# Kernel tuning notes

Hardware: AMD Instinct MI355X
Metric: run time of the kernel (lower is better)

## Reference

```python
import jax, jax.numpy as jnp
import numpy as np

N_MOL = 1024   # molecules
A = 16         # atoms per molecule
N = N_MOL * A  # 16384 atoms
E = N * A      # 262144 edges (all intra-molecule pairs incl. self, box side 2.5 < cutoff 5)
F = 128        # num_features
NRBF = 20
CUT = 5.0
EPS = 1e-8


def _lin(k, fan_in, fan_out):
    kw, kb = jax.random.split(k)
    s = 1.0 / np.sqrt(fan_in)
    return (jax.random.uniform(kw, (fan_in, fan_out), minval=-s, maxval=s),
            jax.random.uniform(kb, (fan_out,), minval=-s, maxval=s))


def setup_inputs() -> dict:
    key = jax.random.key(0)
    ks = jax.random.split(key, 12)
    atoms = jax.random.randint(ks[0], (N,), 0, 100)
    # coordinates in a box of side 2.5 per molecule -> all intra-molecule pairs within cutoff
    atom_positions = jax.random.uniform(ks[1], (N, 3), dtype=jnp.float32) * 2.5
    # deterministic edge list: for each atom i, all atoms j in the same molecule (incl. i itself)
    mol = np.arange(N) // A
    idx_i = jnp.asarray(np.repeat(np.arange(N), A).astype(np.int32))
    idx_j = jnp.asarray(((mol * A)[:, None] + np.arange(A)[None, :]).reshape(-1).astype(np.int32))
    embed = jax.random.normal(ks[2], (100, F), dtype=jnp.float32)
    w_s1, b_s1 = _lin(ks[3], F, F)
    w_s2, b_s2 = _lin(ks[4], F, 3 * F)
    w_r, b_r = _lin(ks[5], NRBF, 3 * F)
    w_u1, b_u1 = _lin(ks[6], 2 * F, F)
    w_u2, b_u2 = _lin(ks[7], F, 3 * F)
    def _lin3(k):
        ws, bs = zip(*[_lin(kk, F, F) for kk in jax.random.split(k, 3)])
        return jnp.stack(ws), jnp.stack(bs)
    Uw, Ub = _lin3(ks[8])   # [3,F,F], [3,F]
    Vw, Vb = _lin3(ks[9])
    return dict(atoms=atoms, atom_positions=atom_positions, idx_i=idx_i, idx_j=idx_j,
                embed=embed, w_s1=w_s1, b_s1=b_s1, w_s2=w_s2, b_s2=b_s2,
                w_r=w_r, b_r=b_r, w_u1=w_u1, b_u1=b_u1, w_u2=w_u2, b_u2=b_u2,
                Uw=Uw, Ub=Ub, Vw=Vw, Vb=Vb)


def reference(atoms, atom_positions, idx_i, idx_j, embed,
              w_s1, b_s1, w_s2, b_s2, w_r, b_r,
              w_u1, b_u1, w_u2, b_u2, Uw, Ub, Vw, Vb):
    silu = jax.nn.silu
    n_nodes = atoms.shape[0]
    s0 = embed[atoms]                                         # [N,F] (v0 is zeros -> its message term vanishes)
    # edge geometry: r_ij = pos_i - pos_j
    rvec = atom_positions[idx_i] - atom_positions[idx_j]      # [E,3]
    d = jnp.linalg.norm(rvec, axis=1, keepdims=True)          # [E,1]
    n = jnp.arange(1, NRBF + 1, dtype=s0.dtype)[None, :]      # [1,20]
    rbf = jnp.sin(n * (jnp.pi / CUT) * d) / (d + EPS)         # [E,20]
    lin_r = rbf @ w_r + b_r                                   # [E,3F]
    # cosine cutoff applied elementwise to the linear output (faithful to source)
    Wg = 0.5 * (jnp.cos(jnp.pi * lin_r / CUT) + 1.0) * (lin_r < CUT).astype(lin_r.dtype)
    phi = silu(s0 @ w_s1 + b_s1) @ w_s2 + b_s2                # [N,3F]
    split = phi[idx_j] * Wg                                   # [E,3F] gather + gate
    split_2 = split[:, F:2 * F]
    split_3 = split[:, 2 * F:]
    unit = rvec / (d + EPS)                                   # [E,3]
    # v_j[js]*split_1 term is identically zero since v_i_0 == 0
    left_2 = split_3[:, :, None] * unit[:, None, :]           # [E,F,3]
    v1 = jnp.zeros((n_nodes, F, 3), dtype=s0.dtype).at[idx_j].add(left_2)
    s1 = jnp.zeros((n_nodes, F), dtype=s0.dtype).at[idx_j].add(split_2)
    # update block: per-spatial-component linear maps
    Uv = jnp.einsum('nik,kio->nok', v1, Uw) + Ub.T[None]      # [N,F,3]
    Vv = jnp.einsum('nik,kio->nok', v1, Vw) + Vb.T[None]
    Vn = jnp.linalg.norm(Vv, axis=2)                          # [N,F]
    m = silu(jnp.concatenate([Vn, s1], axis=1) @ w_u1 + b_u1) @ w_u2 + b_u2
    a_vv, a_sv, a_ss = m[:, :F], m[:, F:2 * F], m[:, 2 * F:]
    delta_v = a_vv[:, :, None] * Uv                           # [N,F,3]
    delta_s = jnp.sum(Uv * Vv, axis=2) * a_sv + a_ss          # [N,F]
    return delta_s, delta_v
```

## Files before the change

kernel.cpp:

```cpp
#include <hip/hip_runtime.h>
#include <stdint.h>

#define N_ATOMS 16384
#define FDIM    128
#define NF      (N_ATOMS * FDIM)
#define PK      136

typedef __bf16 bf16;
typedef bf16  bf16x8 __attribute__((ext_vector_type(8)));
typedef float f32x4  __attribute__((ext_vector_type(4)));

#define MFMA(a, b, c) __builtin_amdgcn_mfma_f32_16x16x32_bf16((a), (b), (c), 0, 0, 0)

__device__ __forceinline__ float silu(float x) { return x / (1.0f + expf(-x)); }

__device__ __forceinline__ uint16_t f2b(float x) {
    union { float f; uint32_t u; } v; v.f = x;
    uint32_t r = (v.u + 0x7FFFu + ((v.u >> 16) & 1u)) >> 16;
    return (uint16_t)r;
}
__device__ __forceinline__ float b2f(uint16_t u) {
    return __uint_as_float(((uint32_t)u) << 16);
}

__device__ __forceinline__ float gate(float lin) {
    float x = lin * 0.1f;
    x = x - floorf(x);
    float cg = 0.5f * (__builtin_amdgcn_cosf(x) + 1.0f);
    return (lin < 5.0f) ? cg : 0.0f;
}

__device__ __forceinline__ void stage_w(uint16_t* bt, const uint16_t* __restrict__ src,
                                        int srcld, int t)
{
    #pragma unroll
    for (int g = 0; g < 8; ++g) {
        int idx = g * 256 + t;
        int n = idx >> 4, q = idx & 15;
        uint4 v = *(const uint4*)(src + (size_t)n * srcld + q * 8);
        *(uint4*)(bt + (size_t)n * PK + q * 8) = v;
    }
}

__global__ __launch_bounds__(256) void prep_kernel(
    const float* __restrict__ w_s1, const float* __restrict__ w_s2,
    const float* __restrict__ w_u1, const float* __restrict__ w_u2,
    const float* __restrict__ Uw,   const float* __restrict__ Vw,
    uint16_t* __restrict__ wb1,  uint16_t* __restrict__ wb2,
    uint16_t* __restrict__ wbu1, uint16_t* __restrict__ wbu2,
    uint16_t* __restrict__ Uwb,  uint16_t* __restrict__ Vwb)
{
    const int e = blockIdx.x * 256 + threadIdx.x;
    switch (blockIdx.y) {
    case 0: {
        if (e < 128 * 128) { int k = e & 127, n = e >> 7;
            wb1[e] = f2b(w_s1[k * 128 + n]); }
        break; }
    case 1: {
        if (e < 256 * 128) { int k = e & 127, n = e >> 7;
            wb2[e] = f2b(w_s2[k * 384 + 128 + n]); }
        break; }
    case 2: {
        if (e < 128 * 256) { int k = e & 255, n = e >> 8;
            wbu1[e] = f2b(w_u1[k * 128 + n]); }
        break; }
    case 3: {
        if (e < 384 * 128) { int k = e & 127, n = e >> 7;
            wbu2[e] = f2b(w_u2[k * 384 + n]); }
        break; }
    case 4: {
        if (e < 384 * 128) { int k = e & 127, n = e >> 7;
            Uwb[e] = f2b(Uw[(n >> 7) * 16384 + k * 128 + (n & 127)]); }
        break; }
    default: {
        if (e < 384 * 128) { int k = e & 127, n = e >> 7;
            Vwb[e] = f2b(Vw[(n >> 7) * 16384 + k * 128 + (n & 127)]); }
        break; }
    }
}

__global__ __launch_bounds__(256) void phi_kernel(
    const int* __restrict__ atoms,
    const float* __restrict__ embed,
    const uint16_t* __restrict__ wb1, const float* __restrict__ b1,
    const uint16_t* __restrict__ wb2, const float* __restrict__ b2,
    uint16_t* __restrict__ phi2)
{
    __shared__ uint16_t aS[64 * PK];
    __shared__ uint16_t bt[128 * PK];
    const int t = threadIdx.x;
    const int w = t >> 6, l = t & 63;
    const int lrow = l & 15, lk = (l >> 4) * 8;
    const int r0 = blockIdx.x * 64;

    {
        const int row = t & 63, ch = (t >> 6) * 32;
        const int aid = atoms[r0 + row];
        const float* src = embed + (size_t)aid * 128 + ch;
        #pragma unroll
        for (int g = 0; g < 4; ++g) {
            float4 v0 = ((const float4*)src)[2 * g];
            float4 v1 = ((const float4*)src)[2 * g + 1];
            union { uint16_t u16[8]; uint4 u4; } pk;
            pk.u16[0] = f2b(v0.x); pk.u16[1] = f2b(v0.y);
            pk.u16[2] = f2b(v0.z); pk.u16[3] = f2b(v0.w);
            pk.u16[4] = f2b(v1.x); pk.u16[5] = f2b(v1.y);
            pk.u16[6] = f2b(v1.z); pk.u16[7] = f2b(v1.w);
            *(uint4*)(aS + (size_t)row * PK + ch + 8 * g) = pk.u4;
        }
    }
    stage_w(bt, wb1, 128, t);
    __syncthreads();

    f32x4 acc1[8];
    #pragma unroll
    for (int n = 0; n < 8; ++n) acc1[n] = f32x4{0.f, 0.f, 0.f, 0.f};
    #pragma unroll
    for (int ks = 0; ks < 128; ks += 32) {
        bf16x8 af = *(const bf16x8*)(aS + (size_t)(16 * w + lrow) * PK + ks + lk);
        #pragma unroll
        for (int n = 0; n < 8; ++n) {
            bf16x8 bfr = *(const bf16x8*)(bt + (size_t)(16 * n + lrow) * PK + ks + lk);
            acc1[n] = MFMA(af, bfr, acc1[n]);
        }
    }
    #pragma unroll
    for (int n = 0; n < 8; ++n) {
        int col = 16 * n + lrow;
        float bb = b1[col];
        #pragma unroll
        for (int i = 0; i < 4; ++i) {
            int rl = 16 * w + (l >> 4) * 4 + i;
            aS[(size_t)rl * PK + col] = f2b(silu(acc1[n][i] + bb));
        }
    }

    for (int cc = 0; cc < 2; ++cc) {
        __syncthreads();
        stage_w(bt, wb2 + (size_t)(128 * cc) * 128, 128, t);
        __syncthreads();
        f32x4 acc[8];
        #pragma unroll
        for (int n = 0; n < 8; ++n) acc[n] = f32x4{0.f, 0.f, 0.f, 0.f};
        #pragma unroll
        for (int ks = 0; ks < 128; ks += 32) {
            bf16x8 af = *(const bf16x8*)(aS + (size_t)(16 * w + lrow) * PK + ks + lk);
            #pragma unroll
            for (int n = 0; n < 8; ++n) {
                bf16x8 bfr = *(const bf16x8*)(bt + (size_t)(16 * n + lrow) * PK + ks + lk);
                acc[n] = MFMA(af, bfr, acc[n]);
            }
        }
        #pragma unroll
        for (int n = 0; n < 8; ++n) {
            int col = 16 * n + lrow;
            float bb = b2[128 + 128 * cc + col];
            #pragma unroll
            for (int i = 0; i < 4; ++i) {
                int row = r0 + 16 * w + (l >> 4) * 4 + i;
                phi2[(size_t)row * 256 + 128 * cc + col] = f2b(acc[n][i] + bb);
            }
        }
    }
}

template <bool NEED_UNIT>
__device__ __forceinline__ void setup_mol(
    const float* __restrict__ pos, int mol0, int t,
    float (&rbf)[120][20], float (&unitv)[120][4],
    int (&pa)[120], int (&pb)[120], float (&posS)[16][3])
{
    if (t < 16) {
        posS[t][0] = pos[(mol0 + t) * 3 + 0];
        posS[t][1] = pos[(mol0 + t) * 3 + 1];
        posS[t][2] = pos[(mol0 + t) * 3 + 2];
    }
    if (t < 120) {
        int p = t;
        int b = (int)(0.5f * (1.0f + sqrtf(8.0f * (float)p + 1.0f)));
        while (b * (b - 1) / 2 > p) --b;
        while ((b + 1) * b / 2 <= p) ++b;
        pa[p] = p - b * (b - 1) / 2;
        pb[p] = b;
    }
    __syncthreads();
    if (t < 120) {
        int a = pa[t], b = pb[t];
        float dx = posS[a][0] - posS[b][0];
        float dy = posS[a][1] - posS[b][1];
        float dz = posS[a][2] - posS[b][2];
        float d = sqrtf(dx * dx + dy * dy + dz * dz);
        float inv = 1.0f / (d + 1e-8f);
        if (NEED_UNIT) {
            unitv[t][0] = dx * inv;
            unitv[t][1] = dy * inv;
            unitv[t][2] = dz * inv;
            unitv[t][3] = 0.f;
        }
        #pragma unroll
        for (int r = 0; r < 20; ++r) {
            float xr = (float)(r + 1) * d * 0.1f;
            xr = xr - floorf(xr);
            rbf[t][r] = __builtin_amdgcn_sinf(xr) * inv;
        }
    }
    __syncthreads();
}

__device__ __forceinline__ float pair_lin(const float (&rbf)[120][20],
                                          const float (&wr)[20], int p, float br)
{
    const float4* rb = (const float4*)&rbf[p][0];
    float lin = br;
    #pragma unroll
    for (int q = 0; q < 5; ++q) {
        float4 rv = rb[q];
        lin += rv.x * wr[4 * q] + rv.y * wr[4 * q + 1]
             + rv.z * wr[4 * q + 2] + rv.w * wr[4 * q + 3];
    }
    return lin;
}

__global__ __launch_bounds__(128) void edge_s2_kernel(
    const float* __restrict__ pos,
    const float* __restrict__ w_r, const float* __restrict__ b_r,
    const uint16_t* __restrict__ phi2,
    uint16_t* __restrict__ Xs)
{
    __shared__ float rbf[120][20];
    __shared__ float unitv[120][4];
    __shared__ int pa[120], pb[120];
    __shared__ float posS[16][3];
    const int t = threadIdx.x;
    const int mol0 = blockIdx.x * 16;
    setup_mol<false>(pos, mol0, t, rbf, unitv, pa, pb, posS);

    const int c = 128 + t;
    float wr[20];
    #pragma unroll
    for (int r = 0; r < 20; ++r) wr[r] = w_r[r * 384 + c];
    const float br = b_r[c];

    float acc[16];
    const float wg0 = gate(br);
    #pragma unroll
    for (int a = 0; a < 16; ++a) acc[a] = wg0;

    #pragma unroll
    for (int b = 1; b < 16; ++b) {
        #pragma unroll
        for (int a = 0; a < b; ++a) {
            const int p = b * (b - 1) / 2 + a;
            float Wg = gate(pair_lin(rbf, wr, p, br));
            acc[a] += Wg;
            acc[b] += Wg;
        }
    }

    #pragma unroll
    for (int a = 0; a < 16; ++a) {
        Xs[(size_t)(mol0 + a) * 128 + t] =
            f2b(b2f(phi2[(size_t)(mol0 + a) * 256 + t]) * acc[a]);
    }
}

__global__ __launch_bounds__(128) void edge_s3_kernel(
    const float* __restrict__ pos,
    const float* __restrict__ w_r, const float* __restrict__ b_r,
    const uint16_t* __restrict__ phi2,
    uint16_t* __restrict__ v1)
{
    __shared__ float rbf[120][20];
    __shared__ float unitv[120][4];
    __shared__ int pa[120], pb[120];
    __shared__ float posS[16][3];
    const int t = threadIdx.x;
    const int mol0 = blockIdx.x * 16;
    setup_mol<true>(pos, mol0, t, rbf, unitv, pa, pb, posS);

    const int c = 256 + t;
    float wr[20];
    #pragma unroll
    for (int r = 0; r < 20; ++r) wr[r] = w_r[r * 384 + c];
    const float br = b_r[c];

    float sx[16], sy[16], sz[16];
    #pragma unroll
    for (int a = 0; a < 16; ++a) { sx[a] = 0.f; sy[a] = 0.f; sz[a] = 0.f; }

    #pragma unroll
    for (int b = 1; b < 16; ++b) {
        #pragma unroll
        for (int a = 0; a < b; ++a) {
            const int p = b * (b - 1) / 2 + a;
            float Wg = gate(pair_lin(rbf, wr, p, br));
            float4 u = *(const float4*)&unitv[p][0];
            float gx = Wg * u.x, gy = Wg * u.y, gz = Wg * u.z;
            sx[b] += gx; sy[b] += gy; sz[b] += gz;
            sx[a] -= gx; sy[a] -= gy; sz[a] -= gz;
        }
    }

    #pragma unroll
    for (int a = 0; a < 16; ++a) {
        float p3 = b2f(phi2[(size_t)(mol0 + a) * 256 + 128 + t]);
        size_t base = (size_t)(mol0 + a) * 128 + t;
        v1[base]                  = f2b(p3 * sx[a]);
        v1[(size_t)NF + base]     = f2b(p3 * sy[a]);
        v1[2 * (size_t)NF + base] = f2b(p3 * sz[a]);
    }
}

__global__ __launch_bounds__(256) void uv_kernel(
    const uint16_t* __restrict__ v1,
    const uint16_t* __restrict__ Uwb, const float* __restrict__ Ub,
    const uint16_t* __restrict__ Vwb, const float* __restrict__ Vb,
    uint16_t* __restrict__ Uvb, uint16_t* __restrict__ Vvb)
{
    __shared__ uint16_t bt[128 * PK];
    const int y = blockIdx.y;
    const int k = y % 3;
    const bool isV = (y >= 3);
    const uint16_t* Bw  = (isV ? Vwb : Uwb) + (size_t)k * 16384;
    const float*   bias = (isV ? Vb : Ub) + k * 128;
    const uint16_t* A = v1 + (size_t)k * NF;
    uint16_t* out = (isV ? Vvb : Uvb) + (size_t)k * NF;

    const int t = threadIdx.x;
    const int w = t >> 6, l = t & 63;
    const int lrow = l & 15, lk = (l >> 4) * 8;
    const int r0 = blockIdx.x * 64;

    stage_w(bt, Bw, 128, t);
    __syncthreads();

    f32x4 acc[8];
    #pragma unroll
    for (int n = 0; n < 8; ++n) acc[n] = f32x4{0.f, 0.f, 0.f, 0.f};

    #pragma unroll
    for (int ks = 0; ks < 128; ks += 32) {
        bf16x8 af = *(const bf16x8*)(A + (size_t)(r0 + 16 * w + lrow) * 128 + ks + lk);
        #pragma unroll
        for (int n = 0; n < 8; ++n) {
            bf16x8 bfr = *(const bf16x8*)(bt + (size_t)(16 * n + lrow) * PK + ks + lk);
            acc[n] = MFMA(af, bfr, acc[n]);
        }
    }

    #pragma unroll
    for (int n = 0; n < 8; ++n) {
        int col = 16 * n + lrow;
        float bb = bias[col];
        #pragma unroll
        for (int i = 0; i < 4; ++i) {
            int row = r0 + 16 * w + (l >> 4) * 4 + i;
            out[(size_t)row * 128 + col] = f2b(acc[n][i] + bb);
        }
    }
}

__global__ __launch_bounds__(256) void update_kernel(
    const uint16_t* __restrict__ Xs,
    const uint16_t* __restrict__ wbu1, const float* __restrict__ b_u1,
    const uint16_t* __restrict__ wbu2, const float* __restrict__ b_u2,
    const uint16_t* __restrict__ Uvb, const uint16_t* __restrict__ Vvb,
    float* __restrict__ out)
{
    __shared__ uint16_t bt[128 * PK];
    __shared__ uint16_t hS[64 * PK];
    const int t = threadIdx.x;
    const int w = t >> 6, l = t & 63;
    const int lrow = l & 15, lk = (l >> 4) * 8;
    const int r0 = blockIdx.x * 64;

    f32x4 acc1[8];
    #pragma unroll
    for (int n = 0; n < 8; ++n) acc1[n] = f32x4{0.f, 0.f, 0.f, 0.f};

    stage_w(bt, wbu1 + 0, 256, t);
    __syncthreads();
    #pragma unroll
    for (int ks = 0; ks < 128; ks += 32) {
        size_t base = (size_t)(r0 + 16 * w + lrow) * 128 + ks + lk;
        uint4 A0 = *(const uint4*)(Vvb + base);
        uint4 A1 = *(const uint4*)(Vvb + (size_t)NF + base);
        uint4 A2 = *(const uint4*)(Vvb + 2 * (size_t)NF + base);
        const uint16_t* p0 = (const uint16_t*)&A0;
        const uint16_t* p1 = (const uint16_t*)&A1;
        const uint16_t* p2 = (const uint16_t*)&A2;
        union { uint16_t u16[8]; bf16x8 v; } af;
        #pragma unroll
        for (int j = 0; j < 8; ++j) {
            float x0 = b2f(p0[j]), x1 = b2f(p1[j]), x2 = b2f(p2[j]);
            af.u16[j] = f2b(sqrtf(x0 * x0 + x1 * x1 + x2 * x2));
        }
        #pragma unroll
        for (int n = 0; n < 8; ++n) {
            bf16x8 bfr = *(const bf16x8*)(bt + (size_t)(16 * n + lrow) * PK + ks + lk);
            acc1[n] = MFMA(af.v, bfr, acc1[n]);
        }
    }

    __syncthreads();
    stage_w(bt, wbu1 + 128, 256, t);
    __syncthreads();
    #pragma unroll
    for (int ks = 0; ks < 128; ks += 32) {
        bf16x8 af = *(const bf16x8*)(Xs + (size_t)(r0 + 16 * w + lrow) * 128 + ks + lk);
        #pragma unroll
        for (int n = 0; n < 8; ++n) {
            bf16x8 bfr = *(const bf16x8*)(bt + (size_t)(16 * n + lrow) * PK + ks + lk);
            acc1[n] = MFMA(af, bfr, acc1[n]);
        }
    }

    #pragma unroll
    for (int n = 0; n < 8; ++n) {
        int col = 16 * n + lrow;
        float bb = b_u1[col];
        #pragma unroll
        for (int i = 0; i < 4; ++i) {
            int rl = 16 * w + (l >> 4) * 4 + i;
            hS[(size_t)rl * PK + col] = f2b(silu(acc1[n][i] + bb));
        }
    }

    f32x4 macc[3][8];
    for (int cc = 0; cc < 3; ++cc) {
        __syncthreads();
        stage_w(bt, wbu2 + (size_t)(128 * cc) * 128, 128, t);
        __syncthreads();
        #pragma unroll
        for (int n = 0; n < 8; ++n) macc[cc][n] = f32x4{0.f, 0.f, 0.f, 0.f};
        #pragma unroll
        for (int ks = 0; ks < 128; ks += 32) {
            bf16x8 af = *(const bf16x8*)(hS + (size_t)(16 * w + lrow) * PK + ks + lk);
            #pragma unroll
            for (int n = 0; n < 8; ++n) {
                bf16x8 bfr = *(const bf16x8*)(bt + (size_t)(16 * n + lrow) * PK + ks + lk);
                macc[cc][n] = MFMA(af, bfr, macc[cc][n]);
            }
        }
    }

    float* dv = out + (size_t)NF;
    #pragma unroll
    for (int n = 0; n < 8; ++n) {
        int f = 16 * n + lrow;
        float bvv = b_u2[f], bsv = b_u2[128 + f], bss = b_u2[256 + f];
        #pragma unroll
        for (int i = 0; i < 4; ++i) {
            int row = r0 + 16 * w + (l >> 4) * 4 + i;
            float a_vv = macc[0][n][i] + bvv;
            float a_sv = macc[1][n][i] + bsv;
            float a_ss = macc[2][n][i] + bss;
            size_t base = (size_t)row * 128 + f;
            float u0 = b2f(Uvb[base]);
            float u1 = b2f(Uvb[(size_t)NF + base]);
            float u2 = b2f(Uvb[2 * (size_t)NF + base]);
            float v0 = b2f(Vvb[base]);
            float v1 = b2f(Vvb[(size_t)NF + base]);
            float v2 = b2f(Vvb[2 * (size_t)NF + base]);
            out[base] = (u0 * v0 + u1 * v1 + u2 * v2) * a_sv + a_ss;
            size_t o = base * 3;
            dv[o + 0] = a_vv * u0;
            dv[o + 1] = a_vv * u1;
            dv[o + 2] = a_vv * u2;
        }
    }
}

extern "C" void kernel_launch(void* const* d_in, const int* in_sizes, int n_in,
                              void* d_out, int out_size, void* d_ws, size_t ws_size,
                              hipStream_t stream)
{
    const int*   atoms = (const int*)d_in[0];
    const float* pos   = (const float*)d_in[1];
    const float* embed = (const float*)d_in[4];
    const float* w_s1  = (const float*)d_in[5];
    const float* b_s1  = (const float*)d_in[6];
    const float* w_s2  = (const float*)d_in[7];
    const float* b_s2  = (const float*)d_in[8];
    const float* w_r   = (const float*)d_in[9];
    const float* b_r   = (const float*)d_in[10];
    const float* w_u1  = (const float*)d_in[11];
    const float* b_u1  = (const float*)d_in[12];
    const float* w_u2  = (const float*)d_in[13];
    const float* b_u2  = (const float*)d_in[14];
    const float* Uw    = (const float*)d_in[15];
    const float* Ub    = (const float*)d_in[16];
    const float* Vw    = (const float*)d_in[17];
    const float* Vb    = (const float*)d_in[18];

    uint16_t* phi2 = (uint16_t*)d_ws;
    uint16_t* Xs   = phi2 + (size_t)N_ATOMS * 256;
    uint16_t* v1b  = Xs   + (size_t)NF;
    uint16_t* Uvb  = v1b  + 3ull * NF;
    uint16_t* Vvb  = Uvb  + 3ull * NF;
    uint16_t* wb1  = Vvb  + 3ull * NF;
    uint16_t* wb2  = wb1  + 128 * 128;
    uint16_t* wbu1 = wb2  + 256 * 128;
    uint16_t* wbu2 = wbu1 + 128 * 256;
    uint16_t* Uwb  = wbu2 + 384 * 128;
    uint16_t* Vwb  = Uwb  + 384 * 128;

    prep_kernel<<<dim3(192, 6), 256, 0, stream>>>(w_s1, w_s2, w_u1, w_u2, Uw, Vw,
                                                  wb1, wb2, wbu1, wbu2, Uwb, Vwb);
    phi_kernel<<<N_ATOMS / 64, 256, 0, stream>>>(atoms, embed, wb1, b_s1, wb2, b_s2, phi2);
    edge_s2_kernel<<<N_ATOMS / 16, 128, 0, stream>>>(pos, w_r, b_r, phi2, Xs);
    edge_s3_kernel<<<N_ATOMS / 16, 128, 0, stream>>>(pos, w_r, b_r, phi2, v1b);
    uv_kernel<<<dim3(N_ATOMS / 64, 6), 256, 0, stream>>>(v1b, Uwb, Ub, Vwb, Vb, Uvb, Vvb);
    update_kernel<<<N_ATOMS / 64, 256, 0, stream>>>(Xs, wbu1, b_u1, wbu2, b_u2, Uvb, Vvb, (float*)d_out);
}
```

Before: 202.8 us.

## Merge edge s2/s3 kernels and halve row tiles in phi and update GEMMs

Combines the two per-molecule edge kernels into one 256-thread kernel, where the first half of the threads computes the scalar-gate sums and the second half the vector sums. This shares the rbf/unit-vector setup and saves a launch. The phi and update kernels now tile 32 rows per block with a 2x2 warp grid instead of 64 rows with 1x4, doubling the block count for better occupancy and load balance, at the cost of restaging the weights twice as often. In the merged edge kernel every thread computes all four accumulators, so each thread does extra work that the other half then discards.

```diff
diff --git a/kernel.cpp b/kernel.cpp
--- a/kernel.cpp
+++ b/kernel.cpp
@@ -86,19 +86,21 @@
     const uint16_t* __restrict__ wb2, const float* __restrict__ b2,
     uint16_t* __restrict__ phi2)
 {
-    __shared__ uint16_t aS[64 * PK];
+    __shared__ uint16_t aS[32 * PK];
     __shared__ uint16_t bt[128 * PK];
     const int t = threadIdx.x;
     const int w = t >> 6, l = t & 63;
-    const int lrow = l & 15, lk = (l >> 4) * 8;
-    const int r0 = blockIdx.x * 64;
+    const int lrow = l & 15, quad = l >> 4, lk = quad * 8;
+    const int rowg = w & 1, colg = w >> 1;
+    const int r0 = blockIdx.x * 32;
 
     {
-        const int row = t & 63, ch = (t >> 6) * 32;
+        const int row = t >> 3;
+        const int ch  = (t & 7) * 16;
         const int aid = atoms[r0 + row];
         const float* src = embed + (size_t)aid * 128 + ch;
         #pragma unroll
-        for (int g = 0; g < 4; ++g) {
+        for (int g = 0; g < 2; ++g) {
             float4 v0 = ((const float4*)src)[2 * g];
             float4 v1 = ((const float4*)src)[2 * g + 1];
             union { uint16_t u16[8]; uint4 u4; } pk;
@@ -112,25 +114,25 @@
     stage_w(bt, wb1, 128, t);
     __syncthreads();
 
-    f32x4 acc1[8];
-    #pragma unroll
-    for (int n = 0; n < 8; ++n) acc1[n] = f32x4{0.f, 0.f, 0.f, 0.f};
+    f32x4 acc1[4];
+    #pragma unroll
+    for (int n = 0; n < 4; ++n) acc1[n] = f32x4{0.f, 0.f, 0.f, 0.f};
     #pragma unroll
     for (int ks = 0; ks < 128; ks += 32) {
-        bf16x8 af = *(const bf16x8*)(aS + (size_t)(16 * w + lrow) * PK + ks + lk);
-        #pragma unroll
-        for (int n = 0; n < 8; ++n) {
-            bf16x8 bfr = *(const bf16x8*)(bt + (size_t)(16 * n + lrow) * PK + ks + lk);
+        bf16x8 af = *(const bf16x8*)(aS + (size_t)(16 * rowg + lrow) * PK + ks + lk);
+        #pragma unroll
+        for (int n = 0; n < 4; ++n) {
+            bf16x8 bfr = *(const bf16x8*)(bt + (size_t)(64 * colg + 16 * n + lrow) * PK + ks + lk);
             acc1[n] = MFMA(af, bfr, acc1[n]);
         }
     }
     #pragma unroll
-    for (int n = 0; n < 8; ++n) {
-        int col = 16 * n + lrow;
+    for (int n = 0; n < 4; ++n) {
+        int col = 64 * colg + 16 * n + lrow;
         float bb = b1[col];
         #pragma unroll
         for (int i = 0; i < 4; ++i) {
-            int rl = 16 * w + (l >> 4) * 4 + i;
+            int rl = 16 * rowg + quad * 4 + i;
             aS[(size_t)rl * PK + col] = f2b(silu(acc1[n][i] + bb));
         }
     }
@@ -139,32 +141,31 @@
         __syncthreads();
         stage_w(bt, wb2 + (size_t)(128 * cc) * 128, 128, t);
         __syncthreads();
-        f32x4 acc[8];
-        #pragma unroll
-        for (int n = 0; n < 8; ++n) acc[n] = f32x4{0.f, 0.f, 0.f, 0.f};
+        f32x4 acc[4];
+        #pragma unroll
+        for (int n = 0; n < 4; ++n) acc[n] = f32x4{0.f, 0.f, 0.f, 0.f};
         #pragma unroll
         for (int ks = 0; ks < 128; ks += 32) {
-            bf16x8 af = *(const bf16x8*)(aS + (size_t)(16 * w + lrow) * PK + ks + lk);
+            bf16x8 af = *(const bf16x8*)(aS + (size_t)(16 * rowg + lrow) * PK + ks + lk);
             #pragma unroll
-            for (int n = 0; n < 8; ++n) {
-                bf16x8 bfr = *(const bf16x8*)(bt + (size_t)(16 * n + lrow) * PK + ks + lk);
+            for (int n = 0; n < 4; ++n) {
+                bf16x8 bfr = *(const bf16x8*)(bt + (size_t)(64 * colg + 16 * n + lrow) * PK + ks + lk);
                 acc[n] = MFMA(af, bfr, acc[n]);
             }
         }
         #pragma unroll
-        for (int n = 0; n < 8; ++n) {
-            int col = 16 * n + lrow;
+        for (int n = 0; n < 4; ++n) {
+            int col = 64 * colg + 16 * n + lrow;
             float bb = b2[128 + 128 * cc + col];
             #pragma unroll
             for (int i = 0; i < 4; ++i) {
-                int row = r0 + 16 * w + (l >> 4) * 4 + i;
+                int row = r0 + 16 * rowg + quad * 4 + i;
                 phi2[(size_t)row * 256 + 128 * cc + col] = f2b(acc[n][i] + bb);
             }
         }
     }
 }
 
-template <bool NEED_UNIT>
 __device__ __forceinline__ void setup_mol(
     const float* __restrict__ pos, int mol0, int t,
     float (&rbf)[120][20], float (&unitv)[120][4],
@@ -191,12 +192,10 @@
         float dz = posS[a][2] - posS[b][2];
         float d = sqrtf(dx * dx + dy * dy + dz * dz);
         float inv = 1.0f / (d + 1e-8f);
-        if (NEED_UNIT) {
-            unitv[t][0] = dx * inv;
-            unitv[t][1] = dy * inv;
-            unitv[t][2] = dz * inv;
-            unitv[t][3] = 0.f;
-        }
+        unitv[t][0] = dx * inv;
+        unitv[t][1] = dy * inv;
+        unitv[t][2] = dz * inv;
+        unitv[t][3] = 0.f;
         #pragma unroll
         for (int r = 0; r < 20; ++r) {
             float xr = (float)(r + 1) * d * 0.1f;
@@ -221,11 +220,12 @@
     return lin;
 }
 
-__global__ __launch_bounds__(128) void edge_s2_kernel(
+__global__ __launch_bounds__(256) void edge_kernel(
     const float* __restrict__ pos,
     const float* __restrict__ w_r, const float* __restrict__ b_r,
     const uint16_t* __restrict__ phi2,
-    uint16_t* __restrict__ Xs)
+    uint16_t* __restrict__ Xs,
+    uint16_t* __restrict__ v1)
 {
     __shared__ float rbf[120][20];
     __shared__ float unitv[120][4];
@@ -233,60 +233,18 @@
     __shared__ float posS[16][3];
     const int t = threadIdx.x;
     const int mol0 = blockIdx.x * 16;
-    setup_mol<false>(pos, mol0, t, rbf, unitv, pa, pb, posS);
+    setup_mol(pos, mol0, t, rbf, unitv, pa, pb, posS);
 
     const int c = 128 + t;
     float wr[20];
     #pragma unroll
     for (int r = 0; r < 20; ++r) wr[r] = w_r[r * 384 + c];
     const float br = b_r[c];
-
-    float acc[16];
-    const float wg0 = gate(br);
-    #pragma unroll
-    for (int a = 0; a < 16; ++a) acc[a] = wg0;
-
-    #pragma unroll
-    for (int b = 1; b < 16; ++b) {
-        #pragma unroll
-        for (int a = 0; a < b; ++a) {
-            const int p = b * (b - 1) / 2 + a;
-            float Wg = gate(pair_lin(rbf, wr, p, br));
-            acc[a] += Wg;
-            acc[b] += Wg;
-        }
-    }
-
-    #pragma unroll
-    for (int a = 0; a < 16; ++a) {
-        Xs[(size_t)(mol0 + a) * 128 + t] =
-            f2b(b2f(phi2[(size_t)(mol0 + a) * 256 + t]) * acc[a]);
-    }
-}
-
-__global__ __launch_bounds__(128) void edge_s3_kernel(
-    const float* __restrict__ pos,
-    const float* __restrict__ w_r, const float* __restrict__ b_r,
-    const uint16_t* __restrict__ phi2,
-    uint16_t* __restrict__ v1)
-{
-    __shared__ float rbf[120][20];
-    __shared__ float unitv[120][4];
-    __shared__ int pa[120], pb[120];
-    __shared__ float posS[16][3];
-    const int t = threadIdx.x;
-    const int mol0 = blockIdx.x * 16;
-    setup_mol<true>(pos, mol0, t, rbf, unitv, pa, pb, posS);
-
-    const int c = 256 + t;
-    float wr[20];
-    #pragma unroll
-    for (int r = 0; r < 20; ++r) wr[r] = w_r[r * 384 + c];
-    const float br = b_r[c];
-
-    float sx[16], sy[16], sz[16];
-    #pragma unroll
-    for (int a = 0; a < 16; ++a) { sx[a] = 0.f; sy[a] = 0.f; sz[a] = 0.f; }
+    const float m = (t < 128) ? 0.f : 1.f;
+
+    float aS[16], aX[16], aY[16], aZ[16];
+    #pragma unroll
+    for (int a = 0; a < 16; ++a) { aS[a] = 0.f; aX[a] = 0.f; aY[a] = 0.f; aZ[a] = 0.f; }
 
     #pragma unroll
     for (int b = 1; b < 16; ++b) {
@@ -295,19 +253,29 @@
             const int p = b * (b - 1) / 2 + a;
             float Wg = gate(pair_lin(rbf, wr, p, br));
             float4 u = *(const float4*)&unitv[p][0];
-            float gx = Wg * u.x, gy = Wg * u.y, gz = Wg * u.z;
-            sx[b] += gx; sy[b] += gy; sz[b] += gz;
-            sx[a] -= gx; sy[a] -= gy; sz[a] -= gz;
-        }
-    }
-
-    #pragma unroll
-    for (int a = 0; a < 16; ++a) {
-        float p3 = b2f(phi2[(size_t)(mol0 + a) * 256 + 128 + t]);
-        size_t base = (size_t)(mol0 + a) * 128 + t;
-        v1[base]                  = f2b(p3 * sx[a]);
-        v1[(size_t)NF + base]     = f2b(p3 * sy[a]);
-        v1[2 * (size_t)NF + base] = f2b(p3 * sz[a]);
+            float gx = Wg * (m * u.x), gy = Wg * (m * u.y), gz = Wg * (m * u.z);
+            aS[b] += Wg;  aX[b] += gx; aY[b] += gy; aZ[b] += gz;
+            aS[a] += Wg;  aX[a] -= gx; aY[a] -= gy; aZ[a] -= gz;
+        }
+    }
+
+    if (t < 128) {
+        const float wg0 = gate(br);
+        #pragma unroll
+        for (int a = 0; a < 16; ++a) {
+            Xs[(size_t)(mol0 + a) * 128 + t] =
+                f2b(b2f(phi2[(size_t)(mol0 + a) * 256 + t]) * (aS[a] + wg0));
+        }
+    } else {
+        const int f = t - 128;
+        #pragma unroll
+        for (int a = 0; a < 16; ++a) {
+            float p3 = b2f(phi2[(size_t)(mol0 + a) * 256 + 128 + f]);
+            size_t base = (size_t)(mol0 + a) * 128 + f;
+            v1[base]                  = f2b(p3 * aX[a]);
+            v1[(size_t)NF + base]     = f2b(p3 * aY[a]);
+            v1[2 * (size_t)NF + base] = f2b(p3 * aZ[a]);
+        }
     }
 }
 
@@ -328,7 +296,7 @@
 
     const int t = threadIdx.x;
     const int w = t >> 6, l = t & 63;
-    const int lrow = l & 15, lk = (l >> 4) * 8;
+    const int lrow = l & 15, quad = l >> 4, lk = quad * 8;
     const int r0 = blockIdx.x * 64;
 
     stage_w(bt, Bw, 128, t);
@@ -354,7 +322,7 @@
         float bb = bias[col];
         #pragma unroll
         for (int i = 0; i < 4; ++i) {
-            int row = r0 + 16 * w + (l >> 4) * 4 + i;
+            int row = r0 + 16 * w + quad * 4 + i;
             out[(size_t)row * 128 + col] = f2b(acc[n][i] + bb);
         }
     }
@@ -368,21 +336,22 @@
     float* __restrict__ out)
 {
     __shared__ uint16_t bt[128 * PK];
-    __shared__ uint16_t hS[64 * PK];
+    __shared__ uint16_t hS[32 * PK];
     const int t = threadIdx.x;
     const int w = t >> 6, l = t & 63;
-    const int lrow = l & 15, lk = (l >> 4) * 8;
-    const int r0 = blockIdx.x * 64;
-
-    f32x4 acc1[8];
-    #pragma unroll
-    for (int n = 0; n < 8; ++n) acc1[n] = f32x4{0.f, 0.f, 0.f, 0.f};
+    const int lrow = l & 15, quad = l >> 4, lk = quad * 8;
+    const int rowg = w & 1, colg = w >> 1;
+    const int r0 = blockIdx.x * 32;
+
+    f32x4 acc1[4];
+    #pragma unroll
+    for (int n = 0; n < 4; ++n) acc1[n] = f32x4{0.f, 0.f, 0.f, 0.f};
 
     stage_w(bt, wbu1 + 0, 256, t);
     __syncthreads();
     #pragma unroll
     for (int ks = 0; ks < 128; ks += 32) {
-        size_t base = (size_t)(r0 + 16 * w + lrow) * 128 + ks + lk;
+        size_t base = (size_t)(r0 + 16 * rowg + lrow) * 128 + ks + lk;
         uint4 A0 = *(const uint4*)(Vvb + base);
         uint4 A1 = *(const uint4*)(Vvb + (size_t)NF + base);
         uint4 A2 = *(const uint4*)(Vvb + 2 * (size_t)NF + base);
@@ -396,8 +365,8 @@
             af.u16[j] = f2b(sqrtf(x0 * x0 + x1 * x1 + x2 * x2));
         }
         #pragma unroll
-        for (int n = 0; n < 8; ++n) {
-            bf16x8 bfr = *(const bf16x8*)(bt + (size_t)(16 * n + lrow) * PK + ks + lk);
+        for (int n = 0; n < 4; ++n) {
+            bf16x8 bfr = *(const bf16x8*)(bt + (size_t)(64 * colg + 16 * n + lrow) * PK + ks + lk);
             acc1[n] = MFMA(af.v, bfr, acc1[n]);
         }
     }
@@ -407,38 +376,38 @@
     __syncthreads();
     #pragma unroll
     for (int ks = 0; ks < 128; ks += 32) {
-        bf16x8 af = *(const bf16x8*)(Xs + (size_t)(r0 + 16 * w + lrow) * 128 + ks + lk);
-        #pragma unroll
-        for (int n = 0; n < 8; ++n) {
-            bf16x8 bfr = *(const bf16x8*)(bt + (size_t)(16 * n + lrow) * PK + ks + lk);
+        bf16x8 af = *(const bf16x8*)(Xs + (size_t)(r0 + 16 * rowg + lrow) * 128 + ks + lk);
+        #pragma unroll
+        for (int n = 0; n < 4; ++n) {
+            bf16x8 bfr = *(const bf16x8*)(bt + (size_t)(64 * colg + 16 * n + lrow) * PK + ks + lk);
             acc1[n] = MFMA(af, bfr, acc1[n]);
         }
     }
 
     #pragma unroll
-    for (int n = 0; n < 8; ++n) {
-        int col = 16 * n + lrow;
+    for (int n = 0; n < 4; ++n) {
+        int col = 64 * colg + 16 * n + lrow;
         float bb = b_u1[col];
         #pragma unroll
         for (int i = 0; i < 4; ++i) {
-            int rl = 16 * w + (l >> 4) * 4 + i;
+            int rl = 16 * rowg + quad * 4 + i;
             hS[(size_t)rl * PK + col] = f2b(silu(acc1[n][i] + bb));
         }
     }
 
-    f32x4 macc[3][8];
+    f32x4 macc[3][4];
     for (int cc = 0; cc < 3; ++cc) {
         __syncthreads();
         stage_w(bt, wbu2 + (size_t)(128 * cc) * 128, 128, t);
         __syncthreads();
         #pragma unroll
-        for (int n = 0; n < 8; ++n) macc[cc][n] = f32x4{0.f, 0.f, 0.f, 0.f};
+        for (int n = 0; n < 4; ++n) macc[cc][n] = f32x4{0.f, 0.f, 0.f, 0.f};
         #pragma unroll
         for (int ks = 0; ks < 128; ks += 32) {
-            bf16x8 af = *(const bf16x8*)(hS + (size_t)(16 * w + lrow) * PK + ks + lk);
+            bf16x8 af = *(const bf16x8*)(hS + (size_t)(16 * rowg + lrow) * PK + ks + lk);
             #pragma unroll
-            for (int n = 0; n < 8; ++n) {
-                bf16x8 bfr = *(const bf16x8*)(bt + (size_t)(16 * n + lrow) * PK + ks + lk);
+            for (int n = 0; n < 4; ++n) {
+                bf16x8 bfr = *(const bf16x8*)(bt + (size_t)(64 * colg + 16 * n + lrow) * PK + ks + lk);
                 macc[cc][n] = MFMA(af, bfr, macc[cc][n]);
             }
         }
@@ -446,12 +415,12 @@
 
     float* dv = out + (size_t)NF;
     #pragma unroll
-    for (int n = 0; n < 8; ++n) {
-        int f = 16 * n + lrow;
+    for (int n = 0; n < 4; ++n) {
+        int f = 64 * colg + 16 * n + lrow;
         float bvv = b_u2[f], bsv = b_u2[128 + f], bss = b_u2[256 + f];
         #pragma unroll
         for (int i = 0; i < 4; ++i) {
-            int row = r0 + 16 * w + (l >> 4) * 4 + i;
+            int row = r0 + 16 * rowg + quad * 4 + i;
             float a_vv = macc[0][n][i] + bvv;
             float a_sv = macc[1][n][i] + bsv;
             float a_ss = macc[2][n][i] + bss;
@@ -507,9 +476,8 @@
 
     prep_kernel<<<dim3(192, 6), 256, 0, stream>>>(w_s1, w_s2, w_u1, w_u2, Uw, Vw,
                                                   wb1, wb2, wbu1, wbu2, Uwb, Vwb);
-    phi_kernel<<<N_ATOMS / 64, 256, 0, stream>>>(atoms, embed, wb1, b_s1, wb2, b_s2, phi2);
-    edge_s2_kernel<<<N_ATOMS / 16, 128, 0, stream>>>(pos, w_r, b_r, phi2, Xs);
-    edge_s3_kernel<<<N_ATOMS / 16, 128, 0, stream>>>(pos, w_r, b_r, phi2, v1b);
+    phi_kernel<<<N_ATOMS / 32, 256, 0, stream>>>(atoms, embed, wb1, b_s1, wb2, b_s2, phi2);
+    edge_kernel<<<N_ATOMS / 16, 256, 0, stream>>>(pos, w_r, b_r, phi2, Xs, v1b);
     uv_kernel<<<dim3(N_ATOMS / 64, 6), 256, 0, stream>>>(v1b, Uwb, Ub, Vwb, Vb, Uvb, Vvb);
-    update_kernel<<<N_ATOMS / 64, 256, 0, stream>>>(Xs, wbu1, b_u1, wbu2, b_u2, Uvb, Vvb, (float*)d_out);
-}
+    update_kernel<<<N_ATOMS / 32, 256, 0, stream>>>(Xs, wbu1, b_u1, wbu2, b_u2, Uvb, Vvb, (float*)d_out);
+}
```

After: 238.4 us. 17.6% more time.

## Fuse edge kernels and compute radial filter and aggregation with MFMA

Applied to the files above, without the earlier changes.

Replaces the two scalar per-feature edge kernels with one fused kernel. Each block builds a bf16 RBF tile per molecule, computes the gated filter for all 120 pairs with MFMA, and performs the per-atom scatter-add of the scalar and vector messages as a second MFMA against a ±1/unit-vector aggregation matrix. This trades scalar FMA work, duplicated geometry setup and an extra launch for tensor-core matmuls. The cost is more bf16 rounding in the filter and in the aggregation coefficients, plus larger shared memory use per block.

```diff
diff --git a/kernel.cpp b/kernel.cpp
--- a/kernel.cpp
+++ b/kernel.cpp
@@ -46,9 +46,11 @@
     const float* __restrict__ w_s1, const float* __restrict__ w_s2,
     const float* __restrict__ w_u1, const float* __restrict__ w_u2,
     const float* __restrict__ Uw,   const float* __restrict__ Vw,
+    const float* __restrict__ w_r,
     uint16_t* __restrict__ wb1,  uint16_t* __restrict__ wb2,
     uint16_t* __restrict__ wbu1, uint16_t* __restrict__ wbu2,
-    uint16_t* __restrict__ Uwb,  uint16_t* __restrict__ Vwb)
+    uint16_t* __restrict__ Uwb,  uint16_t* __restrict__ Vwb,
+    uint16_t* __restrict__ wrbt)
 {
     const int e = blockIdx.x * 256 + threadIdx.x;
     switch (blockIdx.y) {
@@ -72,9 +74,13 @@
         if (e < 384 * 128) { int k = e & 127, n = e >> 7;
             Uwb[e] = f2b(Uw[(n >> 7) * 16384 + k * 128 + (n & 127)]); }
         break; }
-    default: {
+    case 5: {
         if (e < 384 * 128) { int k = e & 127, n = e >> 7;
             Vwb[e] = f2b(Vw[(n >> 7) * 16384 + k * 128 + (n & 127)]); }
+        break; }
+    default: {
+        if (e < 256 * 32) { int k = e & 31, n = e >> 5;
+            wrbt[e] = (k < 20) ? f2b(w_r[k * 384 + 128 + n]) : (uint16_t)0; }
         break; }
     }
 }
@@ -90,7 +96,7 @@
     __shared__ uint16_t bt[128 * PK];
     const int t = threadIdx.x;
     const int w = t >> 6, l = t & 63;
-    const int lrow = l & 15, lk = (l >> 4) * 8;
+    const int lrow = l & 15, quad = l >> 4, lk = quad * 8;
     const int r0 = blockIdx.x * 64;
 
     {
@@ -130,7 +136,7 @@
         float bb = b1[col];
         #pragma unroll
         for (int i = 0; i < 4; ++i) {
-            int rl = 16 * w + (l >> 4) * 4 + i;
+            int rl = 16 * w + quad * 4 + i;
             aS[(size_t)rl * PK + col] = f2b(silu(acc1[n][i] + bb));
         }
     }
@@ -157,157 +163,148 @@
             float bb = b2[128 + 128 * cc + col];
             #pragma unroll
             for (int i = 0; i < 4; ++i) {
-                int row = r0 + 16 * w + (l >> 4) * 4 + i;
+                int row = r0 + 16 * w + quad * 4 + i;
                 phi2[(size_t)row * 256 + 128 * cc + col] = f2b(acc[n][i] + bb);
             }
         }
     }
 }
 
-template <bool NEED_UNIT>
-__device__ __forceinline__ void setup_mol(
-    const float* __restrict__ pos, int mol0, int t,
-    float (&rbf)[120][20], float (&unitv)[120][4],
-    int (&pa)[120], int (&pb)[120], float (&posS)[16][3])
-{
+__global__ __launch_bounds__(256) void edge_kernel(
+    const float* __restrict__ pos,
+    const uint16_t* __restrict__ wrbt,
+    const float* __restrict__ b_r,
+    const uint16_t* __restrict__ phi2,
+    uint16_t* __restrict__ Xs,
+    uint16_t* __restrict__ v1)
+{
+    __shared__ uint16_t rbf_bt[128 * 40];
+    __shared__ uint16_t WgA[128 * PK];
+    __shared__ uint16_t agg[64 * PK];
+    __shared__ float posS[16][3];
+
+    const int t = threadIdx.x;
+    const int w = t >> 6, l = t & 63;
+    const int lrow = l & 15, quad = l >> 4;
+    const int mol0 = blockIdx.x * 16;
+    const uint16_t ONE = 0x3F80;
+
     if (t < 16) {
         posS[t][0] = pos[(mol0 + t) * 3 + 0];
         posS[t][1] = pos[(mol0 + t) * 3 + 1];
         posS[t][2] = pos[(mol0 + t) * 3 + 2];
     }
+    for (int idx = t; idx < 64 * PK / 8; idx += 256)
+        ((uint4*)agg)[idx] = uint4{0, 0, 0, 0};
+    __syncthreads();
+
     if (t < 120) {
         int p = t;
         int b = (int)(0.5f * (1.0f + sqrtf(8.0f * (float)p + 1.0f)));
         while (b * (b - 1) / 2 > p) --b;
         while ((b + 1) * b / 2 <= p) ++b;
-        pa[p] = p - b * (b - 1) / 2;
-        pb[p] = b;
-    }
-    __syncthreads();
-    if (t < 120) {
-        int a = pa[t], b = pb[t];
+        int a = p - b * (b - 1) / 2;
         float dx = posS[a][0] - posS[b][0];
         float dy = posS[a][1] - posS[b][1];
         float dz = posS[a][2] - posS[b][2];
         float d = sqrtf(dx * dx + dy * dy + dz * dz);
         float inv = 1.0f / (d + 1e-8f);
-        if (NEED_UNIT) {
-            unitv[t][0] = dx * inv;
-            unitv[t][1] = dy * inv;
-            unitv[t][2] = dz * inv;
-            unitv[t][3] = 0.f;
-        }
+        float ux = dx * inv, uy = dy * inv, uz = dz * inv;
+
+        union { uint16_t u16[40]; uint4 u4[5]; } row;
         #pragma unroll
         for (int r = 0; r < 20; ++r) {
             float xr = (float)(r + 1) * d * 0.1f;
             xr = xr - floorf(xr);
-            rbf[t][r] = __builtin_amdgcn_sinf(xr) * inv;
-        }
-    }
-    __syncthreads();
-}
-
-__device__ __forceinline__ float pair_lin(const float (&rbf)[120][20],
-                                          const float (&wr)[20], int p, float br)
-{
-    const float4* rb = (const float4*)&rbf[p][0];
-    float lin = br;
-    #pragma unroll
-    for (int q = 0; q < 5; ++q) {
-        float4 rv = rb[q];
-        lin += rv.x * wr[4 * q] + rv.y * wr[4 * q + 1]
-             + rv.z * wr[4 * q + 2] + rv.w * wr[4 * q + 3];
-    }
-    return lin;
-}
-
-__global__ __launch_bounds__(128) void edge_s2_kernel(
-    const float* __restrict__ pos,
-    const float* __restrict__ w_r, const float* __restrict__ b_r,
-    const uint16_t* __restrict__ phi2,
-    uint16_t* __restrict__ Xs)
-{
-    __shared__ float rbf[120][20];
-    __shared__ float unitv[120][4];
-    __shared__ int pa[120], pb[120];
-    __shared__ float posS[16][3];
-    const int t = threadIdx.x;
-    const int mol0 = blockIdx.x * 16;
-    setup_mol<false>(pos, mol0, t, rbf, unitv, pa, pb, posS);
-
-    const int c = 128 + t;
-    float wr[20];
-    #pragma unroll
-    for (int r = 0; r < 20; ++r) wr[r] = w_r[r * 384 + c];
-    const float br = b_r[c];
-
-    float acc[16];
-    const float wg0 = gate(br);
-    #pragma unroll
-    for (int a = 0; a < 16; ++a) acc[a] = wg0;
-
-    #pragma unroll
-    for (int b = 1; b < 16; ++b) {
-        #pragma unroll
-        for (int a = 0; a < b; ++a) {
-            const int p = b * (b - 1) / 2 + a;
-            float Wg = gate(pair_lin(rbf, wr, p, br));
-            acc[a] += Wg;
-            acc[b] += Wg;
-        }
-    }
-
-    #pragma unroll
-    for (int a = 0; a < 16; ++a) {
-        Xs[(size_t)(mol0 + a) * 128 + t] =
-            f2b(b2f(phi2[(size_t)(mol0 + a) * 256 + t]) * acc[a]);
-    }
-}
-
-__global__ __launch_bounds__(128) void edge_s3_kernel(
-    const float* __restrict__ pos,
-    const float* __restrict__ w_r, const float* __restrict__ b_r,
-    const uint16_t* __restrict__ phi2,
-    uint16_t* __restrict__ v1)
-{
-    __shared__ float rbf[120][20];
-    __shared__ float unitv[120][4];
-    __shared__ int pa[120], pb[120];
-    __shared__ float posS[16][3];
-    const int t = threadIdx.x;
-    const int mol0 = blockIdx.x * 16;
-    setup_mol<true>(pos, mol0, t, rbf, unitv, pa, pb, posS);
-
-    const int c = 256 + t;
-    float wr[20];
-    #pragma unroll
-    for (int r = 0; r < 20; ++r) wr[r] = w_r[r * 384 + c];
-    const float br = b_r[c];
-
-    float sx[16], sy[16], sz[16];
-    #pragma unroll
-    for (int a = 0; a < 16; ++a) { sx[a] = 0.f; sy[a] = 0.f; sz[a] = 0.f; }
-
-    #pragma unroll
-    for (int b = 1; b < 16; ++b) {
-        #pragma unroll
-        for (int a = 0; a < b; ++a) {
-            const int p = b * (b - 1) / 2 + a;
-            float Wg = gate(pair_lin(rbf, wr, p, br));
-            float4 u = *(const float4*)&unitv[p][0];
-            float gx = Wg * u.x, gy = Wg * u.y, gz = Wg * u.z;
-            sx[b] += gx; sy[b] += gy; sz[b] += gz;
-            sx[a] -= gx; sy[a] -= gy; sz[a] -= gz;
-        }
-    }
-
-    #pragma unroll
-    for (int a = 0; a < 16; ++a) {
-        float p3 = b2f(phi2[(size_t)(mol0 + a) * 256 + 128 + t]);
-        size_t base = (size_t)(mol0 + a) * 128 + t;
-        v1[base]                  = f2b(p3 * sx[a]);
-        v1[(size_t)NF + base]     = f2b(p3 * sy[a]);
-        v1[2 * (size_t)NF + base] = f2b(p3 * sz[a]);
+            row.u16[r] = f2b(__builtin_amdgcn_sinf(xr) * inv);
+        }
+        #pragma unroll
+        for (int r = 20; r < 40; ++r) row.u16[r] = 0;
+        #pragma unroll
+        for (int g = 0; g < 5; ++g) ((uint4*)(rbf_bt + p * 40))[g] = row.u4[g];
+
+        agg[(0 * 16 + a) * PK + p] = ONE;
+        agg[(0 * 16 + b) * PK + p] = ONE;
+        agg[(16 + a) * PK + p] = f2b(-ux);  agg[(16 + b) * PK + p] = f2b(ux);
+        agg[(32 + a) * PK + p] = f2b(-uy);  agg[(32 + b) * PK + p] = f2b(uy);
+        agg[(48 + a) * PK + p] = f2b(-uz);  agg[(48 + b) * PK + p] = f2b(uz);
+    } else if (t < 128) {
+        #pragma unroll
+        for (int g = 0; g < 5; ++g) ((uint4*)(rbf_bt + t * 40))[g] = uint4{0, 0, 0, 0};
+    } else if (t < 144) {
+        agg[(t - 128) * PK + 120] = ONE;
+    }
+    __syncthreads();
+
+    for (int cc = 0; cc < 2; ++cc) {
+        const uint16_t* wA = wrbt + (size_t)(cc * 128) * 32;
+        #pragma unroll
+        for (int ft2 = 0; ft2 < 2; ++ft2) {
+            const int ft = 2 * w + ft2;
+            bf16x8 afr = *(const bf16x8*)(wA + (size_t)(ft * 16 + lrow) * 32 + quad * 8);
+            float brv[4];
+            #pragma unroll
+            for (int i = 0; i < 4; ++i)
+                brv[i] = b_r[128 + cc * 128 + ft * 16 + quad * 4 + i];
+            #pragma unroll
+            for (int pt = 0; pt < 8; ++pt) {
+                bf16x8 bfr = *(const bf16x8*)(rbf_bt + (size_t)(pt * 16 + lrow) * 40 + quad * 8);
+                f32x4 c = MFMA(afr, bfr, (f32x4{0.f, 0.f, 0.f, 0.f}));
+                #pragma unroll
+                for (int i = 0; i < 4; ++i) {
+                    int f = ft * 16 + quad * 4 + i;
+                    int p = pt * 16 + lrow;
+                    WgA[(size_t)f * PK + p] = f2b(gate(c[i] + brv[i]));
+                }
+            }
+        }
+
+        const int ntiles = cc ? 3 : 1;
+        const int nbase  = cc ? 16 : 0;
+        f32x4 acc[2][3];
+        #pragma unroll
+        for (int ft2 = 0; ft2 < 2; ++ft2)
+            #pragma unroll
+            for (int nt = 0; nt < 3; ++nt) acc[ft2][nt] = f32x4{0.f, 0.f, 0.f, 0.f};
+
+        #pragma unroll
+        for (int ks = 0; ks < 128; ks += 32) {
+            bf16x8 a0 = *(const bf16x8*)(WgA + (size_t)((2 * w) * 16 + lrow) * PK + ks + quad * 8);
+            bf16x8 a1 = *(const bf16x8*)(WgA + (size_t)((2 * w + 1) * 16 + lrow) * PK + ks + quad * 8);
+            for (int nt = 0; nt < ntiles; ++nt) {
+                bf16x8 bfr = *(const bf16x8*)(agg + (size_t)(nbase + nt * 16 + lrow) * PK + ks + quad * 8);
+                acc[0][nt] = MFMA(a0, bfr, acc[0][nt]);
+                acc[1][nt] = MFMA(a1, bfr, acc[1][nt]);
+            }
+        }
+
+        const int a = lrow;
+        #pragma unroll
+        for (int ft2 = 0; ft2 < 2; ++ft2) {
+            const int fbase = (2 * w + ft2) * 16 + quad * 4;
+            float ph[4];
+            #pragma unroll
+            for (int i = 0; i < 4; ++i)
+                ph[i] = b2f(phi2[(size_t)(mol0 + a) * 256 + cc * 128 + fbase + i]);
+            if (cc == 0) {
+                ushort4 ov;
+                ov.x = f2b(ph[0] * acc[ft2][0][0]);
+                ov.y = f2b(ph[1] * acc[ft2][0][1]);
+                ov.z = f2b(ph[2] * acc[ft2][0][2]);
+                ov.w = f2b(ph[3] * acc[ft2][0][3]);
+                *(ushort4*)(Xs + (size_t)(mol0 + a) * 128 + fbase) = ov;
+            } else {
+                #pragma unroll
+                for (int nt = 0; nt < 3; ++nt) {
+                    ushort4 ov;
+                    ov.x = f2b(ph[0] * acc[ft2][nt][0]);
+                    ov.y = f2b(ph[1] * acc[ft2][nt][1]);
+                    ov.z = f2b(ph[2] * acc[ft2][nt][2]);
+                    ov.w = f2b(ph[3] * acc[ft2][nt][3]);
+                    *(ushort4*)(v1 + (size_t)nt * NF + (size_t)(mol0 + a) * 128 + fbase) = ov;
+                }
+            }
+        }
     }
 }
 
@@ -328,7 +325,7 @@
 
     const int t = threadIdx.x;
     const int w = t >> 6, l = t & 63;
-    const int lrow = l & 15, lk = (l >> 4) * 8;
+    const int lrow = l & 15, quad = l >> 4, lk = quad * 8;
     const int r0 = blockIdx.x * 64;
 
     stage_w(bt, Bw, 128, t);
@@ -354,7 +351,7 @@
         float bb = bias[col];
         #pragma unroll
         for (int i = 0; i < 4; ++i) {
-            int row = r0 + 16 * w + (l >> 4) * 4 + i;
+            int row = r0 + 16 * w + quad * 4 + i;
             out[(size_t)row * 128 + col] = f2b(acc[n][i] + bb);
         }
     }
@@ -371,7 +368,7 @@
     __shared__ uint16_t hS[64 * PK];
     const int t = threadIdx.x;
     const int w = t >> 6, l = t & 63;
-    const int lrow = l & 15, lk = (l >> 4) * 8;
+    const int lrow = l & 15, quad = l >> 4, lk = quad * 8;
     const int r0 = blockIdx.x * 64;
 
     f32x4 acc1[8];
@@ -421,7 +418,7 @@
         float bb = b_u1[col];
         #pragma unroll
         for (int i = 0; i < 4; ++i) {
-            int rl = 16 * w + (l >> 4) * 4 + i;
+            int rl = 16 * w + quad * 4 + i;
             hS[(size_t)rl * PK + col] = f2b(silu(acc1[n][i] + bb));
         }
     }
@@ -451,7 +448,7 @@
         float bvv = b_u2[f], bsv = b_u2[128 + f], bss = b_u2[256 + f];
         #pragma unroll
         for (int i = 0; i < 4; ++i) {
-            int row = r0 + 16 * w + (l >> 4) * 4 + i;
+            int row = r0 + 16 * w + quad * 4 + i;
             float a_vv = macc[0][n][i] + bvv;
             float a_sv = macc[1][n][i] + bsv;
             float a_ss = macc[2][n][i] + bss;
@@ -504,12 +501,12 @@
     uint16_t* wbu2 = wbu1 + 128 * 256;
     uint16_t* Uwb  = wbu2 + 384 * 128;
     uint16_t* Vwb  = Uwb  + 384 * 128;
-
-    prep_kernel<<<dim3(192, 6), 256, 0, stream>>>(w_s1, w_s2, w_u1, w_u2, Uw, Vw,
-                                                  wb1, wb2, wbu1, wbu2, Uwb, Vwb);
+    uint16_t* wrbt = Vwb  + 384 * 128;
+
+    prep_kernel<<<dim3(192, 7), 256, 0, stream>>>(w_s1, w_s2, w_u1, w_u2, Uw, Vw, w_r,
+                                                  wb1, wb2, wbu1, wbu2, Uwb, Vwb, wrbt);
     phi_kernel<<<N_ATOMS / 64, 256, 0, stream>>>(atoms, embed, wb1, b_s1, wb2, b_s2, phi2);
-    edge_s2_kernel<<<N_ATOMS / 16, 128, 0, stream>>>(pos, w_r, b_r, phi2, Xs);
-    edge_s3_kernel<<<N_ATOMS / 16, 128, 0, stream>>>(pos, w_r, b_r, phi2, v1b);
+    edge_kernel<<<N_ATOMS / 16, 256, 0, stream>>>(pos, wrbt, b_r, phi2, Xs, v1b);
     uv_kernel<<<dim3(N_ATOMS / 64, 6), 256, 0, stream>>>(v1b, Uwb, Ub, Vwb, Vb, Uvb, Vvb);
     update_kernel<<<N_ATOMS / 64, 256, 0, stream>>>(Xs, wbu1, b_u1, wbu2, b_u2, Uvb, Vvb, (float*)d_out);
 }
```

Measured after the change: 175.0 us. 1.16x faster.
